# Kernel tuning notes

Measured on AMD Instinct MI355X. Metric: run time of the kernel, lower is better.

Reference implementation:

```python
import jax, jax.numpy as jnp
import numpy as np

N = 50000
E = 800000
NFEAT, NHID, NCLASS = 128, 128, 40


def setup_inputs() -> dict:
    key = jax.random.key(0)
    ks = jax.random.split(key, 8)
    x = jax.random.normal(ks[0], (N, NFEAT), dtype=jnp.float32)
    edge_index = jax.random.randint(ks[1], (2, E), 0, N, dtype=jnp.int64)
    def glorot(k, fan_in, fan_out):
        s = jnp.sqrt(6.0 / (fan_in + fan_out)).astype(jnp.float32)
        return jax.random.uniform(k, (fan_in, fan_out), jnp.float32, -s, s)
    W1 = glorot(ks[2], NFEAT, NHID); b1 = jnp.zeros((NHID,), jnp.float32)
    W2 = glorot(ks[3], NHID, NHID);  b2 = jnp.zeros((NHID,), jnp.float32)
    W3 = glorot(ks[4], NHID, NCLASS); b3 = jnp.zeros((NCLASS,), jnp.float32)
    return {"x": x, "edge_index": edge_index,
            "W1": W1, "b1": b1, "W2": W2, "b2": b2, "W3": W3, "b3": b3}


def _gcn_norm(edge_index, num_nodes, dtype):
    # Add self-loops, then symmetric normalization D^-1/2 (A+I) D^-1/2 (PyG gcn_norm).
    loop = jnp.arange(num_nodes, dtype=edge_index.dtype)
    src = jnp.concatenate([edge_index[0], loop])
    dst = jnp.concatenate([edge_index[1], loop])
    deg = jax.ops.segment_sum(jnp.ones_like(src, dtype=dtype), dst, num_segments=num_nodes)
    dinv = jnp.where(deg > 0, deg ** -0.5, 0.0).astype(dtype)
    norm = dinv[src] * dinv[dst]  # [E+N]
    return src, dst, norm


def _gcn_conv(h, src, dst, norm, W, b, num_nodes):
    h = h @ W                              # dense transform first (out_dim small)
    msg = h[src] * norm[:, None]           # gather + per-edge scale
    out = jax.ops.segment_sum(msg, dst, num_segments=num_nodes)  # scatter-add
    return out + b


def reference(x, edge_index, W1, b1, W2, b2, W3, b3):
    src, dst, norm = _gcn_norm(edge_index, N, x.dtype)
    h = jax.nn.relu(_gcn_conv(x, src, dst, norm, W1, b1, N))  # dropout: eval mode (identity)
    h = jax.nn.relu(_gcn_conv(h, src, dst, norm, W2, b2, N))
    h = _gcn_conv(h, src, dst, norm, W3, b3, N)
    return jax.nn.log_softmax(h, axis=-1)
```

## Files before the change

### kernel.cpp

```cpp
#include <hip/hip_runtime.h>
#include <stdint.h>

#define NN 50000
#define NE 800000
#define GG 782
#define NB 196
#define TT 2048
#define SB 391
#define SLAB 8192

typedef __attribute__((ext_vector_type(8))) short bfx8;
typedef __attribute__((ext_vector_type(4))) float f32x4;

__device__ inline unsigned short f2bf(float f) {
    union { float f; uint32_t u; } x; x.f = f;
    uint32_t u = x.u;
    return (unsigned short)((u + 0x7fffu + ((u >> 16) & 1u)) >> 16);
}
__device__ inline uint32_t pack2bf(float lo, float hi) {
    return (uint32_t)f2bf(lo) | ((uint32_t)f2bf(hi) << 16);
}
__device__ inline float bf2f(unsigned short h) {
    union { uint32_t u; float f; } c; c.u = ((uint32_t)h) << 16;
    return c.f;
}
__device__ inline float2 bfp2f2(uint32_t v) {
    union { uint32_t u; float f; } a, b;
    a.u = (v & 0xffffu) << 16;
    b.u = v & 0xffff0000u;
    return make_float2(a.f, b.f);
}
__device__ inline bfx8 ld8(const unsigned short* p) {
    union { uint4 u; bfx8 v; } c;
    c.u = *(const uint4*)p;
    return c.v;
}
__device__ inline bfx8 cvt8(float4 u, float4 v) {
    union { unsigned short s[8]; bfx8 r; } c;
    c.s[0] = f2bf(u.x); c.s[1] = f2bf(u.y); c.s[2] = f2bf(u.z); c.s[3] = f2bf(u.w);
    c.s[4] = f2bf(v.x); c.s[5] = f2bf(v.y); c.s[6] = f2bf(v.z); c.s[7] = f2bf(v.w);
    return c.r;
}

__global__ void prep(const float* __restrict__ W1, const float* __restrict__ W2,
                     const float* __restrict__ W3,
                     unsigned short* __restrict__ WT1, unsigned short* __restrict__ WT2,
                     unsigned short* __restrict__ WT3, int* __restrict__ cursor) {
    if (blockIdx.x == 152) {
        if (threadIdx.x < NB) cursor[threadIdx.x] = 0;
        return;
    }
    int w = blockIdx.x * 256 + threadIdx.x;
    if (w < 16384) {
        int nn = w >> 7, k = w & 127;
        WT1[nn * 128 + k] = f2bf(W1[k * 128 + nn]);
    } else if (w < 32768) {
        int w2 = w - 16384, nn = w2 >> 7, k = w2 & 127;
        WT2[nn * 128 + k] = f2bf(W2[k * 128 + nn]);
    } else if (w < 38912) {
        int w2 = w - 32768, nn = w2 >> 7, k = w2 & 127;
        WT3[nn * 128 + k] = (nn < 40) ? f2bf(W3[k * 40 + nn]) : (unsigned short)0;
    }
}

__global__ __launch_bounds__(256) void gemm1_hist(const float* __restrict__ X,
                                                  const unsigned short* __restrict__ WT,
                                                  unsigned short* __restrict__ G, int n,
                                                  const int* __restrict__ src,
                                                  const int* __restrict__ dst,
                                                  int* __restrict__ cursor,
                                                  uint32_t* __restrict__ packA, int e) {
    __shared__ int lc[NB];
    __shared__ int gb[NB];
    if (blockIdx.x >= GG) {
        int b = blockIdx.x - GG;
        int t = threadIdx.x;
        if (t < NB) lc[t] = 0;
        __syncthreads();
        int start = b * TT;
        int end = start + TT; if (end > e) end = e;
        int hi_[8], r_[8];
        uint32_t pk_[8];
#pragma unroll
        for (int j = 0; j < 8; j++) {
            int i = start + j * 256 + t;
            if (i < end) {
                int dd = dst[i], ss = src[i];
                hi_[j] = dd >> 8;
                pk_[j] = ((uint32_t)dd << 16) | (uint32_t)ss;
                r_[j] = atomicAdd(&lc[hi_[j]], 1);
            } else r_[j] = -1;
        }
        __syncthreads();
        if (t < NB) {
            int c = lc[t];
            gb[t] = c ? atomicAdd(&cursor[t], c) : 0;
        }
        __syncthreads();
#pragma unroll
        for (int j = 0; j < 8; j++) {
            if (r_[j] >= 0)
                packA[(size_t)hi_[j] * SLAB + gb[hi_[j]] + r_[j]] = pk_[j];
        }
        return;
    }
    int wave = threadIdx.x >> 6;
    int lane = threadIdx.x & 63;
    int quad = lane >> 4;
    int c = lane & 15;
    int rowbase = blockIdx.x * 64 + wave * 16;

    int arow = rowbase + c;
    if (arow >= n) arow = n - 1;
    const float* ap = X + (size_t)arow * 128 + quad * 8;
    bfx8 a[4];
#pragma unroll
    for (int kc = 0; kc < 4; kc++) {
        float4 u = *(const float4*)(ap + kc * 32);
        float4 v = *(const float4*)(ap + kc * 32 + 4);
        a[kc] = cvt8(u, v);
    }

    f32x4 acc[8];
#pragma unroll
    for (int ct = 0; ct < 8; ct++) acc[ct] = (f32x4){0.f, 0.f, 0.f, 0.f};
#pragma unroll
    for (int ct = 0; ct < 8; ct++) {
        const unsigned short* bp = WT + (size_t)(ct * 16 + c) * 128 + quad * 8;
#pragma unroll
        for (int kc = 0; kc < 4; kc++) {
            bfx8 b = ld8(bp + kc * 32);
            acc[ct] = __builtin_amdgcn_mfma_f32_16x16x32_bf16(a[kc], b, acc[ct], 0, 0, 0);
        }
    }

    int r0 = rowbase + quad * 4;
    bool odd = lane & 1;
#pragma unroll
    for (int ct = 0; ct < 8; ct++) {
        float x0 = acc[ct][0], x1 = acc[ct][1], x2 = acc[ct][2], x3 = acc[ct][3];
        float y0 = __shfl_xor(x0, 1, 64), y1 = __shfl_xor(x1, 1, 64);
        float y2 = __shfl_xor(x2, 1, 64), y3 = __shfl_xor(x3, 1, 64);
        int colp = ct * 16 + (c & ~1);
        if (!odd) {
            if (r0 + 0 < n) *(uint32_t*)(&G[(size_t)(r0 + 0) * 128 + colp]) = pack2bf(x0, y0);
            if (r0 + 1 < n) *(uint32_t*)(&G[(size_t)(r0 + 1) * 128 + colp]) = pack2bf(x1, y1);
        } else {
            if (r0 + 2 < n) *(uint32_t*)(&G[(size_t)(r0 + 2) * 128 + colp]) = pack2bf(y2, x2);
            if (r0 + 3 < n) *(uint32_t*)(&G[(size_t)(r0 + 3) * 128 + colp]) = pack2bf(y3, x3);
        }
    }
}

__global__ __launch_bounds__(256) void buildB(const uint32_t* __restrict__ packA,
                                              const int* __restrict__ cursor,
                                              int* __restrict__ row_ptr, int* __restrict__ deg,
                                              float* __restrict__ dinv,
                                              unsigned short* __restrict__ csr_src, int n) {
    __shared__ int s[256];
    __shared__ int cnt[256];
    __shared__ int rp[256];
    __shared__ int basehi, bcnt;
    int hi = blockIdx.x;
    int t = threadIdx.x;
    int bc = (t < NB) ? cursor[t] : 0;
    s[t] = bc;
    __syncthreads();
#pragma unroll
    for (int off = 1; off < 256; off <<= 1) {
        int y = (t >= off) ? s[t - off] : 0;
        __syncthreads();
        s[t] += y;
        __syncthreads();
    }
    if (t == hi) { basehi = s[t] - bc; bcnt = bc; }
    cnt[t] = 0;
    __syncthreads();
    int b0 = basehi;
    int mc = bcnt;
    const uint32_t* slab = packA + (size_t)hi * SLAB;
    for (int i = t; i < mc; i += 256)
        atomicAdd(&cnt[(slab[i] >> 16) & 0xFF], 1);
    __syncthreads();
    int v = cnt[t];
    s[t] = v;
    __syncthreads();
#pragma unroll
    for (int off = 1; off < 256; off <<= 1) {
        int y = (t >= off) ? s[t - off] : 0;
        __syncthreads();
        s[t] += y;
        __syncthreads();
    }
    rp[t] = b0 + s[t] - v;
    int node = hi * 256 + t;
    if (node < n) {
        row_ptr[node] = rp[t];
        deg[node] = v;
        dinv[node] = rsqrtf(1.0f + (float)v);
    }
    cnt[t] = 0;
    __syncthreads();
    for (int i = t; i < mc; i += 256) {
        uint32_t p = slab[i];
        int lo = (p >> 16) & 0xFF;
        int r = atomicAdd(&cnt[lo], 1);
        csr_src[rp[lo] + r] = (unsigned short)(p & 0xFFFF);
    }
}

__global__ __launch_bounds__(256) void gemm128_mfma(const unsigned short* __restrict__ A,
                                                    const unsigned short* __restrict__ WT,
                                                    const float* __restrict__ dinv,
                                                    unsigned short* __restrict__ G, int n) {
    int wave = threadIdx.x >> 6;
    int lane = threadIdx.x & 63;
    int quad = lane >> 4;
    int c = lane & 15;
    int rowbase = blockIdx.x * 64 + wave * 16;

    int arow = rowbase + c;
    if (arow >= n) arow = n - 1;
    const unsigned short* ap = A + (size_t)arow * 128 + quad * 8;
    bfx8 a[4];
#pragma unroll
    for (int kc = 0; kc < 4; kc++) a[kc] = ld8(ap + kc * 32);

    f32x4 acc[8];
#pragma unroll
    for (int ct = 0; ct < 8; ct++) acc[ct] = (f32x4){0.f, 0.f, 0.f, 0.f};
#pragma unroll
    for (int ct = 0; ct < 8; ct++) {
        const unsigned short* bp = WT + (size_t)(ct * 16 + c) * 128 + quad * 8;
#pragma unroll
        for (int kc = 0; kc < 4; kc++) {
            bfx8 b = ld8(bp + kc * 32);
            acc[ct] = __builtin_amdgcn_mfma_f32_16x16x32_bf16(a[kc], b, acc[ct], 0, 0, 0);
        }
    }

    int r0 = rowbase + quad * 4;
    float di[4];
#pragma unroll
    for (int r = 0; r < 4; r++) {
        int rr = r0 + r;
        di[r] = dinv[rr < n ? rr : 0];
    }
    bool odd = lane & 1;
#pragma unroll
    for (int ct = 0; ct < 8; ct++) {
        float x0 = acc[ct][0], x1 = acc[ct][1], x2 = acc[ct][2], x3 = acc[ct][3];
        float y0 = __shfl_xor(x0, 1, 64), y1 = __shfl_xor(x1, 1, 64);
        float y2 = __shfl_xor(x2, 1, 64), y3 = __shfl_xor(x3, 1, 64);
        int colp = ct * 16 + (c & ~1);
        if (!odd) {
            if (r0 + 0 < n) *(uint32_t*)(&G[(size_t)(r0 + 0) * 128 + colp]) = pack2bf(di[0] * x0, di[0] * y0);
            if (r0 + 1 < n) *(uint32_t*)(&G[(size_t)(r0 + 1) * 128 + colp]) = pack2bf(di[1] * x1, di[1] * y1);
        } else {
            if (r0 + 2 < n) *(uint32_t*)(&G[(size_t)(r0 + 2) * 128 + colp]) = pack2bf(di[2] * y2, di[2] * x2);
            if (r0 + 3 < n) *(uint32_t*)(&G[(size_t)(r0 + 3) * 128 + colp]) = pack2bf(di[3] * y3, di[3] * x3);
        }
    }
}

__global__ __launch_bounds__(256) void gemm40_mfma(const unsigned short* __restrict__ A,
                                                   const unsigned short* __restrict__ WT,
                                                   const float* __restrict__ dinv,
                                                   unsigned short* __restrict__ G, int n) {
    int wave = threadIdx.x >> 6;
    int lane = threadIdx.x & 63;
    int quad = lane >> 4;
    int c = lane & 15;
    int rowbase = blockIdx.x * 64 + wave * 16;

    int arow = rowbase + c;
    if (arow >= n) arow = n - 1;
    const unsigned short* ap = A + (size_t)arow * 128 + quad * 8;
    bfx8 a[4];
#pragma unroll
    for (int kc = 0; kc < 4; kc++) a[kc] = ld8(ap + kc * 32);

    f32x4 acc[3];
#pragma unroll
    for (int ct = 0; ct < 3; ct++) acc[ct] = (f32x4){0.f, 0.f, 0.f, 0.f};
#pragma unroll
    for (int ct = 0; ct < 3; ct++) {
        const unsigned short* bp = WT + (size_t)(ct * 16 + c) * 128 + quad * 8;
#pragma unroll
        for (int kc = 0; kc < 4; kc++) {
            bfx8 b = ld8(bp + kc * 32);
            acc[ct] = __builtin_amdgcn_mfma_f32_16x16x32_bf16(a[kc], b, acc[ct], 0, 0, 0);
        }
    }

    int r0 = rowbase + quad * 4;
    float di[4];
#pragma unroll
    for (int r = 0; r < 4; r++) {
        int rr = r0 + r;
        di[r] = dinv[rr < n ? rr : 0];
    }
    bool odd = lane & 1;
#pragma unroll
    for (int ct = 0; ct < 3; ct++) {
        float x0 = acc[ct][0], x1 = acc[ct][1], x2 = acc[ct][2], x3 = acc[ct][3];
        float y0 = __shfl_xor(x0, 1, 64), y1 = __shfl_xor(x1, 1, 64);
        float y2 = __shfl_xor(x2, 1, 64), y3 = __shfl_xor(x3, 1, 64);
        int colp = ct * 16 + (c & ~1);
        if (colp >= 40) continue;
        if (!odd) {
            if (r0 + 0 < n) *(uint32_t*)(&G[(size_t)(r0 + 0) * 40 + colp]) = pack2bf(di[0] * x0, di[0] * y0);
            if (r0 + 1 < n) *(uint32_t*)(&G[(size_t)(r0 + 1) * 40 + colp]) = pack2bf(di[1] * x1, di[1] * y1);
        } else {
            if (r0 + 2 < n) *(uint32_t*)(&G[(size_t)(r0 + 2) * 40 + colp]) = pack2bf(di[2] * y2, di[2] * x2);
            if (r0 + 3 < n) *(uint32_t*)(&G[(size_t)(r0 + 3) * 40 + colp]) = pack2bf(di[3] * y3, di[3] * x3);
        }
    }
}

__global__ __launch_bounds__(256) void agg128_l1(const unsigned short* __restrict__ G,
                                                 const int* __restrict__ row_ptr,
                                                 const int* __restrict__ deg,
                                                 const unsigned short* __restrict__ csr_src,
                                                 const float* __restrict__ dinv,
                                                 const float* __restrict__ b,
                                                 unsigned short* __restrict__ Y, int n) {
    int node = blockIdx.x * 4 + (threadIdx.x >> 6);
    if (node >= n) return;
    int l = threadIdx.x & 63;
    int h = l >> 5, fl = l & 31;
    const uint2* Gr = (const uint2*)G;

    float dn = dinv[node];
    float4 acc = make_float4(0.f, 0.f, 0.f, 0.f);
    if (h == 0) {
        uint2 sq = Gr[(size_t)node * 32 + fl];
        float2 a0 = bfp2f2(sq.x), a1 = bfp2f2(sq.y);
        acc = make_float4(dn * a0.x, dn * a0.y, dn * a1.x, dn * a1.y);
    }
    int p = row_ptr[node];
    int p1 = p + deg[node];
    for (int q = p; q < p1; q += 8) {
        int i0 = q + h, i1 = q + 2 + h, i2 = q + 4 + h, i3 = q + 6 + h;
        bool v0 = i0 < p1, v1 = i1 < p1, v2 = i2 < p1, v3 = i3 < p1;
        int s0 = csr_src[v0 ? i0 : p], s1 = csr_src[v1 ? i1 : p];
        int s2 = csr_src[v2 ? i2 : p], s3 = csr_src[v3 ? i3 : p];
        float d0 = v0 ? dinv[s0] : 0.f, d1 = v1 ? dinv[s1] : 0.f;
        float d2 = v2 ? dinv[s2] : 0.f, d3 = v3 ? dinv[s3] : 0.f;
        uint2 q0 = Gr[(size_t)s0 * 32 + fl], q1 = Gr[(size_t)s1 * 32 + fl];
        uint2 q2 = Gr[(size_t)s2 * 32 + fl], q3 = Gr[(size_t)s3 * 32 + fl];
        float2 x0 = bfp2f2(q0.x), y0 = bfp2f2(q0.y);
        float2 x1 = bfp2f2(q1.x), y1 = bfp2f2(q1.y);
        float2 x2 = bfp2f2(q2.x), y2 = bfp2f2(q2.y);
        float2 x3 = bfp2f2(q3.x), y3 = bfp2f2(q3.y);
        acc.x += fmaf(d0, x0.x, d1 * x1.x) + fmaf(d2, x2.x, d3 * x3.x);
        acc.y += fmaf(d0, x0.y, d1 * x1.y) + fmaf(d2, x2.y, d3 * x3.y);
        acc.z += fmaf(d0, y0.x, d1 * y1.x) + fmaf(d2, y2.x, d3 * y3.x);
        acc.w += fmaf(d0, y0.y, d1 * y1.y) + fmaf(d2, y2.y, d3 * y3.y);
    }
    acc.x += __shfl_xor(acc.x, 32, 64);
    acc.y += __shfl_xor(acc.y, 32, 64);
    acc.z += __shfl_xor(acc.z, 32, 64);
    acc.w += __shfl_xor(acc.w, 32, 64);
    float4 bb = ((const float4*)b)[fl];
    float r0 = fmaf(dn, acc.x, bb.x);
    float r1 = fmaf(dn, acc.y, bb.y);
    float r2 = fmaf(dn, acc.z, bb.z);
    float r3 = fmaf(dn, acc.w, bb.w);
    if (h == 0) {
        uint2 o;
        o.x = pack2bf(r0 > 0.f ? r0 : 0.f, r1 > 0.f ? r1 : 0.f);
        o.y = pack2bf(r2 > 0.f ? r2 : 0.f, r3 > 0.f ? r3 : 0.f);
        ((uint2*)Y)[(size_t)node * 32 + fl] = o;
    }
}

__global__ __launch_bounds__(256) void agg128(const unsigned short* __restrict__ G,
                                              const int* __restrict__ row_ptr,
                                              const int* __restrict__ deg,
                                              const unsigned short* __restrict__ csr_src,
                                              const float* __restrict__ dinv,
                                              const float* __restrict__ b,
                                              unsigned short* __restrict__ Y, int n) {
    int node = blockIdx.x * 4 + (threadIdx.x >> 6);
    if (node >= n) return;
    int l = threadIdx.x & 63;
    int h = l >> 5, fl = l & 31;
    const uint2* Gr = (const uint2*)G;

    float4 acc = make_float4(0.f, 0.f, 0.f, 0.f);
    if (h == 0) {
        uint2 sq = Gr[(size_t)node * 32 + fl];
        float2 a0 = bfp2f2(sq.x), a1 = bfp2f2(sq.y);
        acc = make_float4(a0.x, a0.y, a1.x, a1.y);
    }
    int p = row_ptr[node];
    int p1 = p + deg[node];
    for (int q = p; q < p1; q += 8) {
        int i0 = q + h, i1 = q + 2 + h, i2 = q + 4 + h, i3 = q + 6 + h;
        bool v0 = i0 < p1, v1 = i1 < p1, v2 = i2 < p1, v3 = i3 < p1;
        int s0 = csr_src[v0 ? i0 : p], s1 = csr_src[v1 ? i1 : p];
        int s2 = csr_src[v2 ? i2 : p], s3 = csr_src[v3 ? i3 : p];
        float d0 = v0 ? 1.f : 0.f, d1 = v1 ? 1.f : 0.f;
        float d2 = v2 ? 1.f : 0.f, d3 = v3 ? 1.f : 0.f;
        uint2 q0 = Gr[(size_t)s0 * 32 + fl], q1 = Gr[(size_t)s1 * 32 + fl];
        uint2 q2 = Gr[(size_t)s2 * 32 + fl], q3 = Gr[(size_t)s3 * 32 + fl];
        float2 x0 = bfp2f2(q0.x), y0 = bfp2f2(q0.y);
        float2 x1 = bfp2f2(q1.x), y1 = bfp2f2(q1.y);
        float2 x2 = bfp2f2(q2.x), y2 = bfp2f2(q2.y);
        float2 x3 = bfp2f2(q3.x), y3 = bfp2f2(q3.y);
        acc.x += fmaf(d0, x0.x, d1 * x1.x) + fmaf(d2, x2.x, d3 * x3.x);
        acc.y += fmaf(d0, x0.y, d1 * x1.y) + fmaf(d2, x2.y, d3 * x3.y);
        acc.z += fmaf(d0, y0.x, d1 * y1.x) + fmaf(d2, y2.x, d3 * y3.x);
        acc.w += fmaf(d0, y0.y, d1 * y1.y) + fmaf(d2, y2.y, d3 * y3.y);
    }
    acc.x += __shfl_xor(acc.x, 32, 64);
    acc.y += __shfl_xor(acc.y, 32, 64);
    acc.z += __shfl_xor(acc.z, 32, 64);
    acc.w += __shfl_xor(acc.w, 32, 64);
    float dn = dinv[node];
    float4 bb = ((const float4*)b)[fl];
    float r0 = fmaf(dn, acc.x, bb.x);
    float r1 = fmaf(dn, acc.y, bb.y);
    float r2 = fmaf(dn, acc.z, bb.z);
    float r3 = fmaf(dn, acc.w, bb.w);
    if (h == 0) {
        uint2 o;
        o.x = pack2bf(r0 > 0.f ? r0 : 0.f, r1 > 0.f ? r1 : 0.f);
        o.y = pack2bf(r2 > 0.f ? r2 : 0.f, r3 > 0.f ? r3 : 0.f);
        ((uint2*)Y)[(size_t)node * 32 + fl] = o;
    }
}

__global__ __launch_bounds__(256) void agg40_lsm(const unsigned short* __restrict__ G,
                                                 const int* __restrict__ row_ptr,
                                                 const int* __restrict__ deg,
                                                 const unsigned short* __restrict__ csr_src,
                                                 const float* __restrict__ dinv,
                                                 const float* __restrict__ b,
                                                 float* __restrict__ Y, int n) {
    int node = blockIdx.x * 4 + (threadIdx.x >> 6);
    if (node >= n) return;
    int l = threadIdx.x & 63;
    int h = l >> 5, fl = l & 31;
    bool act = fl < 10;
    int flc = act ? fl : 0;
    const uint2* Gr = (const uint2*)G;

    float4 acc = make_float4(0.f, 0.f, 0.f, 0.f);
    if (h == 0) {
        uint2 sq = Gr[(size_t)node * 10 + flc];
        float2 a0 = bfp2f2(sq.x), a1 = bfp2f2(sq.y);
        acc = make_float4(a0.x, a0.y, a1.x, a1.y);
    }
    int p = row_ptr[node];
    int p1 = p + deg[node];
    for (int q = p; q < p1; q += 8) {
        int i0 = q + h, i1 = q + 2 + h, i2 = q + 4 + h, i3 = q + 6 + h;
        bool v0 = i0 < p1, v1 = i1 < p1, v2 = i2 < p1, v3 = i3 < p1;
        int s0 = csr_src[v0 ? i0 : p], s1 = csr_src[v1 ? i1 : p];
        int s2 = csr_src[v2 ? i2 : p], s3 = csr_src[v3 ? i3 : p];
        float d0 = v0 ? 1.f : 0.f, d1 = v1 ? 1.f : 0.f;
        float d2 = v2 ? 1.f : 0.f, d3 = v3 ? 1.f : 0.f;
        uint2 q0 = Gr[(size_t)s0 * 10 + flc], q1 = Gr[(size_t)s1 * 10 + flc];
        uint2 q2 = Gr[(size_t)s2 * 10 + flc], q3 = Gr[(size_t)s3 * 10 + flc];
        float2 x0 = bfp2f2(q0.x), y0 = bfp2f2(q0.y);
        float2 x1 = bfp2f2(q1.x), y1 = bfp2f2(q1.y);
        float2 x2 = bfp2f2(q2.x), y2 = bfp2f2(q2.y);
        float2 x3 = bfp2f2(q3.x), y3 = bfp2f2(q3.y);
        acc.x += fmaf(d0, x0.x, d1 * x1.x) + fmaf(d2, x2.x, d3 * x3.x);
        acc.y += fmaf(d0, x0.y, d1 * x1.y) + fmaf(d2, x2.y, d3 * x3.y);
        acc.z += fmaf(d0, y0.x, d1 * y1.x) + fmaf(d2, y2.x, d3 * y3.x);
        acc.w += fmaf(d0, y0.y, d1 * y1.y) + fmaf(d2, y2.y, d3 * y3.y);
    }
    acc.x += __shfl_xor(acc.x, 32, 64);
    acc.y += __shfl_xor(acc.y, 32, 64);
    acc.z += __shfl_xor(acc.z, 32, 64);
    acc.w += __shfl_xor(acc.w, 32, 64);
    float dn = dinv[node];
    const float4* b4 = (const float4*)b;
    float4 bb = b4[flc];
    float v0_ = fmaf(dn, acc.x, bb.x);
    float v1_ = fmaf(dn, acc.y, bb.y);
    float v2_ = fmaf(dn, acc.z, bb.z);
    float v3_ = fmaf(dn, acc.w, bb.w);
    float m = act ? fmaxf(fmaxf(v0_, v1_), fmaxf(v2_, v3_)) : -1e30f;
#pragma unroll
    for (int off = 8; off > 0; off >>= 1) m = fmaxf(m, __shfl_xor(m, off, 16));
    float e0 = act ? expf(v0_ - m) : 0.f;
    float e1 = act ? expf(v1_ - m) : 0.f;
    float e2 = act ? expf(v2_ - m) : 0.f;
    float e3 = act ? expf(v3_ - m) : 0.f;
    float s_ = ((e0 + e1) + (e2 + e3));
#pragma unroll
    for (int off = 8; off > 0; off >>= 1) s_ += __shfl_xor(s_, off, 16);
    float ls = logf(s_) + m;
    if (h == 0 && act) {
        float4 o = make_float4(v0_ - ls, v1_ - ls, v2_ - ls, v3_ - ls);
        ((float4*)Y)[(size_t)node * 10 + fl] = o;
    }
}


extern "C" void kernel_launch(void* const* d_in, const int* in_sizes, int n_in,
                              void* d_out, int out_size, void* d_ws, size_t ws_size,
                              hipStream_t stream) {
    const float* x  = (const float*)d_in[0];
    const int*   ei = (const int*)d_in[1];
    const float* W1 = (const float*)d_in[2];
    const float* b1 = (const float*)d_in[3];
    const float* W2 = (const float*)d_in[4];
    const float* b2 = (const float*)d_in[5];
    const float* W3 = (const float*)d_in[6];
    const float* b3 = (const float*)d_in[7];
    float* out = (float*)d_out;

    const int n = NN, e = NE;
    const int* srcI = ei;
    const int* dstI = ei + e;

    char* ws = (char*)d_ws;
    int*            deg     = (int*)ws;
    int*            row_ptr = (int*)(ws + 200704);
    float*          dinv    = (float*)(ws + 401408);
    int*            cursor  = (int*)(ws + 602112);
    uint32_t*       packA   = (uint32_t*)(ws + 603136);
    unsigned short* csr_src = (unsigned short*)(ws + 7025664);
    unsigned short* WT1     = (unsigned short*)(ws + 8625664);
    unsigned short* WT2     = (unsigned short*)(ws + 8658432);
    unsigned short* WT3     = (unsigned short*)(ws + 8691200);
    unsigned short* bufG    = (unsigned short*)(ws + 8703488);
    unsigned short* bufA    = (unsigned short*)(ws + 21503488);

    prep<<<153, 256, 0, stream>>>(W1, W2, W3, WT1, WT2, WT3, cursor);
    gemm1_hist<<<GG + SB, 256, 0, stream>>>(x, WT1, bufG, n, srcI, dstI, cursor, packA, e);
    buildB<<<NB, 256, 0, stream>>>(packA, cursor, row_ptr, deg, dinv, csr_src, n);
    agg128_l1<<<(n + 3) / 4, 256, 0, stream>>>(bufG, row_ptr, deg, csr_src, dinv, b1, bufA, n);
    gemm128_mfma<<<GG, 256, 0, stream>>>(bufA, WT2, dinv, bufG, n);
    agg128<<<(n + 3) / 4, 256, 0, stream>>>(bufG, row_ptr, deg, csr_src, dinv, b2, bufA, n);
    gemm40_mfma<<<GG, 256, 0, stream>>>(bufA, WT3, dinv, bufG, n);
    agg40_lsm<<<(n + 3) / 4, 256, 0, stream>>>(bufG, row_ptr, deg, csr_src, dinv, b3, out, n);
}
```

Before: 271.1 us.

## Store 128-wide features in column slabs so aggregation gathers stay cache-resident

The 128-feature intermediate buffers become four 32-column slabs, each a contiguous array of 64-byte rows. The GEMMs write and read that slab layout, and the 128-wide aggregation kernels now launch four times as many blocks. Each block handles one slab for a group of nodes, interleaved so a slab's working set (about 3.2 MB) can stay in L2 during the random neighbour gathers. The cost is a fourfold re-read of the CSR indices and dinv, narrower 64-byte gathers, and a longer shuffle reduction across eight edge slots.

```diff
diff --git a/kernel.cpp b/kernel.cpp
--- a/kernel.cpp
+++ b/kernel.cpp
@@ -3,11 +3,16 @@
 
 #define NN 50000
 #define NE 800000
+#define NRP 50048
 #define GG 782
 #define NB 196
 #define TT 2048
 #define SB 391
 #define SLAB 8192
+#define SLABE (NRP * 32)
+#define SLABU (NRP * 16)
+#define SLABU2 (NRP * 8)
+#define AGGB 50000
 
 typedef __attribute__((ext_vector_type(8))) short bfx8;
 typedef __attribute__((ext_vector_type(4))) float f32x4;
@@ -136,18 +141,20 @@
 
     int r0 = rowbase + quad * 4;
     bool odd = lane & 1;
+    uint32_t* Gu = (uint32_t*)G;
 #pragma unroll
     for (int ct = 0; ct < 8; ct++) {
         float x0 = acc[ct][0], x1 = acc[ct][1], x2 = acc[ct][2], x3 = acc[ct][3];
         float y0 = __shfl_xor(x0, 1, 64), y1 = __shfl_xor(x1, 1, 64);
         float y2 = __shfl_xor(x2, 1, 64), y3 = __shfl_xor(x3, 1, 64);
         int colp = ct * 16 + (c & ~1);
+        size_t sbase = (size_t)(colp >> 5) * SLABU + ((colp & 31) >> 1);
         if (!odd) {
-            if (r0 + 0 < n) *(uint32_t*)(&G[(size_t)(r0 + 0) * 128 + colp]) = pack2bf(x0, y0);
-            if (r0 + 1 < n) *(uint32_t*)(&G[(size_t)(r0 + 1) * 128 + colp]) = pack2bf(x1, y1);
+            if (r0 + 0 < n) Gu[sbase + (size_t)(r0 + 0) * 16] = pack2bf(x0, y0);
+            if (r0 + 1 < n) Gu[sbase + (size_t)(r0 + 1) * 16] = pack2bf(x1, y1);
         } else {
-            if (r0 + 2 < n) *(uint32_t*)(&G[(size_t)(r0 + 2) * 128 + colp]) = pack2bf(y2, x2);
-            if (r0 + 3 < n) *(uint32_t*)(&G[(size_t)(r0 + 3) * 128 + colp]) = pack2bf(y3, x3);
+            if (r0 + 2 < n) Gu[sbase + (size_t)(r0 + 2) * 16] = pack2bf(y2, x2);
+            if (r0 + 3 < n) Gu[sbase + (size_t)(r0 + 3) * 16] = pack2bf(y3, x3);
         }
     }
 }
@@ -221,10 +228,10 @@
 
     int arow = rowbase + c;
     if (arow >= n) arow = n - 1;
-    const unsigned short* ap = A + (size_t)arow * 128 + quad * 8;
+    const unsigned short* ap = A + (size_t)arow * 32 + quad * 8;
     bfx8 a[4];
 #pragma unroll
-    for (int kc = 0; kc < 4; kc++) a[kc] = ld8(ap + kc * 32);
+    for (int kc = 0; kc < 4; kc++) a[kc] = ld8(ap + (size_t)kc * SLABE);
 
     f32x4 acc[8];
 #pragma unroll
@@ -247,18 +254,20 @@
         di[r] = dinv[rr < n ? rr : 0];
     }
     bool odd = lane & 1;
+    uint32_t* Gu = (uint32_t*)G;
 #pragma unroll
     for (int ct = 0; ct < 8; ct++) {
         float x0 = acc[ct][0], x1 = acc[ct][1], x2 = acc[ct][2], x3 = acc[ct][3];
         float y0 = __shfl_xor(x0, 1, 64), y1 = __shfl_xor(x1, 1, 64);
         float y2 = __shfl_xor(x2, 1, 64), y3 = __shfl_xor(x3, 1, 64);
         int colp = ct * 16 + (c & ~1);
+        size_t sbase = (size_t)(colp >> 5) * SLABU + ((colp & 31) >> 1);
         if (!odd) {
-            if (r0 + 0 < n) *(uint32_t*)(&G[(size_t)(r0 + 0) * 128 + colp]) = pack2bf(di[0] * x0, di[0] * y0);
-            if (r0 + 1 < n) *(uint32_t*)(&G[(size_t)(r0 + 1) * 128 + colp]) = pack2bf(di[1] * x1, di[1] * y1);
+            if (r0 + 0 < n) Gu[sbase + (size_t)(r0 + 0) * 16] = pack2bf(di[0] * x0, di[0] * y0);
+            if (r0 + 1 < n) Gu[sbase + (size_t)(r0 + 1) * 16] = pack2bf(di[1] * x1, di[1] * y1);
         } else {
-            if (r0 + 2 < n) *(uint32_t*)(&G[(size_t)(r0 + 2) * 128 + colp]) = pack2bf(di[2] * y2, di[2] * x2);
-            if (r0 + 3 < n) *(uint32_t*)(&G[(size_t)(r0 + 3) * 128 + colp]) = pack2bf(di[3] * y3, di[3] * x3);
+            if (r0 + 2 < n) Gu[sbase + (size_t)(r0 + 2) * 16] = pack2bf(di[2] * y2, di[2] * x2);
+            if (r0 + 3 < n) Gu[sbase + (size_t)(r0 + 3) * 16] = pack2bf(di[3] * y3, di[3] * x3);
         }
     }
 }
@@ -275,10 +284,10 @@
 
     int arow = rowbase + c;
     if (arow >= n) arow = n - 1;
-    const unsigned short* ap = A + (size_t)arow * 128 + quad * 8;
+    const unsigned short* ap = A + (size_t)arow * 32 + quad * 8;
     bfx8 a[4];
 #pragma unroll
-    for (int kc = 0; kc < 4; kc++) a[kc] = ld8(ap + kc * 32);
+    for (int kc = 0; kc < 4; kc++) a[kc] = ld8(ap + (size_t)kc * SLABE);
 
     f32x4 acc[3];
 #pragma unroll
@@ -325,53 +334,55 @@
                                                  const float* __restrict__ dinv,
                                                  const float* __restrict__ b,
                                                  unsigned short* __restrict__ Y, int n) {
-    int node = blockIdx.x * 4 + (threadIdx.x >> 6);
+    int bi = blockIdx.x;
+    int xs = bi & 7;
+    int slab = xs >> 1;
+    int grp = (bi >> 3) * 2 + (xs & 1);
+    int node = grp * 4 + (threadIdx.x >> 6);
     if (node >= n) return;
     int l = threadIdx.x & 63;
-    int h = l >> 5, fl = l & 31;
-    const uint2* Gr = (const uint2*)G;
+    int slot = l >> 3, f = l & 7;
+    const uint2* Gs = (const uint2*)G + (size_t)slab * SLABU2;
 
     float dn = dinv[node];
     float4 acc = make_float4(0.f, 0.f, 0.f, 0.f);
-    if (h == 0) {
-        uint2 sq = Gr[(size_t)node * 32 + fl];
-        float2 a0 = bfp2f2(sq.x), a1 = bfp2f2(sq.y);
-        acc = make_float4(dn * a0.x, dn * a0.y, dn * a1.x, dn * a1.y);
-    }
     int p = row_ptr[node];
     int p1 = p + deg[node];
     for (int q = p; q < p1; q += 8) {
-        int i0 = q + h, i1 = q + 2 + h, i2 = q + 4 + h, i3 = q + 6 + h;
-        bool v0 = i0 < p1, v1 = i1 < p1, v2 = i2 < p1, v3 = i3 < p1;
-        int s0 = csr_src[v0 ? i0 : p], s1 = csr_src[v1 ? i1 : p];
-        int s2 = csr_src[v2 ? i2 : p], s3 = csr_src[v3 ? i3 : p];
-        float d0 = v0 ? dinv[s0] : 0.f, d1 = v1 ? dinv[s1] : 0.f;
-        float d2 = v2 ? dinv[s2] : 0.f, d3 = v3 ? dinv[s3] : 0.f;
-        uint2 q0 = Gr[(size_t)s0 * 32 + fl], q1 = Gr[(size_t)s1 * 32 + fl];
-        uint2 q2 = Gr[(size_t)s2 * 32 + fl], q3 = Gr[(size_t)s3 * 32 + fl];
-        float2 x0 = bfp2f2(q0.x), y0 = bfp2f2(q0.y);
-        float2 x1 = bfp2f2(q1.x), y1 = bfp2f2(q1.y);
-        float2 x2 = bfp2f2(q2.x), y2 = bfp2f2(q2.y);
-        float2 x3 = bfp2f2(q3.x), y3 = bfp2f2(q3.y);
-        acc.x += fmaf(d0, x0.x, d1 * x1.x) + fmaf(d2, x2.x, d3 * x3.x);
-        acc.y += fmaf(d0, x0.y, d1 * x1.y) + fmaf(d2, x2.y, d3 * x3.y);
-        acc.z += fmaf(d0, y0.x, d1 * y1.x) + fmaf(d2, y2.x, d3 * y3.x);
-        acc.w += fmaf(d0, y0.y, d1 * y1.y) + fmaf(d2, y2.y, d3 * y3.y);
-    }
-    acc.x += __shfl_xor(acc.x, 32, 64);
-    acc.y += __shfl_xor(acc.y, 32, 64);
-    acc.z += __shfl_xor(acc.z, 32, 64);
-    acc.w += __shfl_xor(acc.w, 32, 64);
-    float4 bb = ((const float4*)b)[fl];
+        int i = q + slot;
+        bool v = i < p1;
+        int s = csr_src[v ? i : p];
+        float d = v ? dinv[s] : 0.f;
+        uint2 r = Gs[(size_t)s * 8 + f];
+        float2 lo = bfp2f2(r.x), hi = bfp2f2(r.y);
+        acc.x = fmaf(d, lo.x, acc.x);
+        acc.y = fmaf(d, lo.y, acc.y);
+        acc.z = fmaf(d, hi.x, acc.z);
+        acc.w = fmaf(d, hi.y, acc.w);
+    }
+#pragma unroll
+    for (int off = 8; off < 64; off <<= 1) {
+        acc.x += __shfl_xor(acc.x, off, 64);
+        acc.y += __shfl_xor(acc.y, off, 64);
+        acc.z += __shfl_xor(acc.z, off, 64);
+        acc.w += __shfl_xor(acc.w, off, 64);
+    }
+    uint2 sr = Gs[(size_t)node * 8 + f];
+    float2 slo = bfp2f2(sr.x), shi = bfp2f2(sr.y);
+    acc.x = fmaf(dn, slo.x, acc.x);
+    acc.y = fmaf(dn, slo.y, acc.y);
+    acc.z = fmaf(dn, shi.x, acc.z);
+    acc.w = fmaf(dn, shi.y, acc.w);
+    float4 bb = ((const float4*)b)[slab * 8 + f];
     float r0 = fmaf(dn, acc.x, bb.x);
     float r1 = fmaf(dn, acc.y, bb.y);
     float r2 = fmaf(dn, acc.z, bb.z);
     float r3 = fmaf(dn, acc.w, bb.w);
-    if (h == 0) {
+    if (slot == 0) {
         uint2 o;
         o.x = pack2bf(r0 > 0.f ? r0 : 0.f, r1 > 0.f ? r1 : 0.f);
         o.y = pack2bf(r2 > 0.f ? r2 : 0.f, r3 > 0.f ? r3 : 0.f);
-        ((uint2*)Y)[(size_t)node * 32 + fl] = o;
+        ((uint2*)Y)[(size_t)slab * SLABU2 + (size_t)node * 8 + f] = o;
     }
 }
 
@@ -382,53 +393,52 @@
                                               const float* __restrict__ dinv,
                                               const float* __restrict__ b,
                                               unsigned short* __restrict__ Y, int n) {
-    int node = blockIdx.x * 4 + (threadIdx.x >> 6);
+    int bi = blockIdx.x;
+    int xs = bi & 7;
+    int slab = xs >> 1;
+    int grp = (bi >> 3) * 2 + (xs & 1);
+    int node = grp * 4 + (threadIdx.x >> 6);
     if (node >= n) return;
     int l = threadIdx.x & 63;
-    int h = l >> 5, fl = l & 31;
-    const uint2* Gr = (const uint2*)G;
+    int slot = l >> 3, f = l & 7;
+    const uint2* Gs = (const uint2*)G + (size_t)slab * SLABU2;
 
     float4 acc = make_float4(0.f, 0.f, 0.f, 0.f);
-    if (h == 0) {
-        uint2 sq = Gr[(size_t)node * 32 + fl];
-        float2 a0 = bfp2f2(sq.x), a1 = bfp2f2(sq.y);
-        acc = make_float4(a0.x, a0.y, a1.x, a1.y);
-    }
     int p = row_ptr[node];
     int p1 = p + deg[node];
     for (int q = p; q < p1; q += 8) {
-        int i0 = q + h, i1 = q + 2 + h, i2 = q + 4 + h, i3 = q + 6 + h;
-        bool v0 = i0 < p1, v1 = i1 < p1, v2 = i2 < p1, v3 = i3 < p1;
-        int s0 = csr_src[v0 ? i0 : p], s1 = csr_src[v1 ? i1 : p];
-        int s2 = csr_src[v2 ? i2 : p], s3 = csr_src[v3 ? i3 : p];
-        float d0 = v0 ? 1.f : 0.f, d1 = v1 ? 1.f : 0.f;
-        float d2 = v2 ? 1.f : 0.f, d3 = v3 ? 1.f : 0.f;
-        uint2 q0 = Gr[(size_t)s0 * 32 + fl], q1 = Gr[(size_t)s1 * 32 + fl];
-        uint2 q2 = Gr[(size_t)s2 * 32 + fl], q3 = Gr[(size_t)s3 * 32 + fl];
-        float2 x0 = bfp2f2(q0.x), y0 = bfp2f2(q0.y);
-        float2 x1 = bfp2f2(q1.x), y1 = bfp2f2(q1.y);
-        float2 x2 = bfp2f2(q2.x), y2 = bfp2f2(q2.y);
-        float2 x3 = bfp2f2(q3.x), y3 = bfp2f2(q3.y);
-        acc.x += fmaf(d0, x0.x, d1 * x1.x) + fmaf(d2, x2.x, d3 * x3.x);
-        acc.y += fmaf(d0, x0.y, d1 * x1.y) + fmaf(d2, x2.y, d3 * x3.y);
-        acc.z += fmaf(d0, y0.x, d1 * y1.x) + fmaf(d2, y2.x, d3 * y3.x);
-        acc.w += fmaf(d0, y0.y, d1 * y1.y) + fmaf(d2, y2.y, d3 * y3.y);
-    }
-    acc.x += __shfl_xor(acc.x, 32, 64);
-    acc.y += __shfl_xor(acc.y, 32, 64);
-    acc.z += __shfl_xor(acc.z, 32, 64);
-    acc.w += __shfl_xor(acc.w, 32, 64);
+        int i = q + slot;
+        bool v = i < p1;
+        int s = csr_src[v ? i : p];
+        float d = v ? 1.f : 0.f;
+        uint2 r = Gs[(size_t)s * 8 + f];
+        float2 lo = bfp2f2(r.x), hi = bfp2f2(r.y);
+        acc.x = fmaf(d, lo.x, acc.x);
+        acc.y = fmaf(d, lo.y, acc.y);
+        acc.z = fmaf(d, hi.x, acc.z);
+        acc.w = fmaf(d, hi.y, acc.w);
+    }
+#pragma unroll
+    for (int off = 8; off < 64; off <<= 1) {
+        acc.x += __shfl_xor(acc.x, off, 64);
+        acc.y += __shfl_xor(acc.y, off, 64);
+        acc.z += __shfl_xor(acc.z, off, 64);
+        acc.w += __shfl_xor(acc.w, off, 64);
+    }
+    uint2 sr = Gs[(size_t)node * 8 + f];
+    float2 slo = bfp2f2(sr.x), shi = bfp2f2(sr.y);
+    acc.x += slo.x; acc.y += slo.y; acc.z += shi.x; acc.w += shi.y;
     float dn = dinv[node];
-    float4 bb = ((const float4*)b)[fl];
+    float4 bb = ((const float4*)b)[slab * 8 + f];
     float r0 = fmaf(dn, acc.x, bb.x);
     float r1 = fmaf(dn, acc.y, bb.y);
     float r2 = fmaf(dn, acc.z, bb.z);
     float r3 = fmaf(dn, acc.w, bb.w);
-    if (h == 0) {
+    if (slot == 0) {
         uint2 o;
         o.x = pack2bf(r0 > 0.f ? r0 : 0.f, r1 > 0.f ? r1 : 0.f);
         o.y = pack2bf(r2 > 0.f ? r2 : 0.f, r3 > 0.f ? r3 : 0.f);
-        ((uint2*)Y)[(size_t)node * 32 + fl] = o;
+        ((uint2*)Y)[(size_t)slab * SLABU2 + (size_t)node * 8 + f] = o;
     }
 }
 
@@ -530,14 +540,14 @@
     unsigned short* WT2     = (unsigned short*)(ws + 8658432);
     unsigned short* WT3     = (unsigned short*)(ws + 8691200);
     unsigned short* bufG    = (unsigned short*)(ws + 8703488);
-    unsigned short* bufA    = (unsigned short*)(ws + 21503488);
+    unsigned short* bufA    = (unsigned short*)(ws + 21515776);
 
     prep<<<153, 256, 0, stream>>>(W1, W2, W3, WT1, WT2, WT3, cursor);
     gemm1_hist<<<GG + SB, 256, 0, stream>>>(x, WT1, bufG, n, srcI, dstI, cursor, packA, e);
     buildB<<<NB, 256, 0, stream>>>(packA, cursor, row_ptr, deg, dinv, csr_src, n);
-    agg128_l1<<<(n + 3) / 4, 256, 0, stream>>>(bufG, row_ptr, deg, csr_src, dinv, b1, bufA, n);
+    agg128_l1<<<AGGB, 256, 0, stream>>>(bufG, row_ptr, deg, csr_src, dinv, b1, bufA, n);
     gemm128_mfma<<<GG, 256, 0, stream>>>(bufA, WT2, dinv, bufG, n);
-    agg128<<<(n + 3) / 4, 256, 0, stream>>>(bufG, row_ptr, deg, csr_src, dinv, b2, bufA, n);
+    agg128<<<AGGB, 256, 0, stream>>>(bufG, row_ptr, deg, csr_src, dinv, b2, bufA, n);
     gemm40_mfma<<<GG, 256, 0, stream>>>(bufA, WT3, dinv, bufG, n);
     agg40_lsm<<<(n + 3) / 4, 256, 0, stream>>>(bufG, row_ptr, deg, csr_src, dinv, b3, out, n);
 }
```

Result: slower. 357.1 us (+31.8%).

## Fold layer-1 dinv prescale into buildB and unroll agg128 to 16 edges

Applied to the files above, without the earlier changes.

The layer-1 GEMM output is now scaled in place by each node's dinv inside buildB, which already holds the per-node degrees in shared memory. This lets layer 1 reuse the generic agg128 kernel and drops the per-edge dinv[src] gathers from agg128_l1. Separately, the agg128 edge loop now issues up to 16 neighbor gathers per iteration to get more loads in flight, at the cost of more registers. It also adds an extra bf16 rounding of layer-1 features and a read-modify-write pass over them inside buildB.

```diff
diff --git a/kernel.cpp b/kernel.cpp
--- a/kernel.cpp
+++ b/kernel.cpp
@@ -156,10 +156,12 @@
                                               const int* __restrict__ cursor,
                                               int* __restrict__ row_ptr, int* __restrict__ deg,
                                               float* __restrict__ dinv,
-                                              unsigned short* __restrict__ csr_src, int n) {
+                                              unsigned short* __restrict__ csr_src,
+                                              unsigned short* __restrict__ G, int n) {
     __shared__ int s[256];
     __shared__ int cnt[256];
     __shared__ int rp[256];
+    __shared__ float sdinv[256];
     __shared__ int basehi, bcnt;
     int hi = blockIdx.x;
     int t = threadIdx.x;
@@ -193,11 +195,13 @@
         __syncthreads();
     }
     rp[t] = b0 + s[t] - v;
+    float dv = rsqrtf(1.0f + (float)v);
+    sdinv[t] = dv;
     int node = hi * 256 + t;
     if (node < n) {
         row_ptr[node] = rp[t];
         deg[node] = v;
-        dinv[node] = rsqrtf(1.0f + (float)v);
+        dinv[node] = dv;
     }
     cnt[t] = 0;
     __syncthreads();
@@ -206,6 +210,23 @@
         int lo = (p >> 16) & 0xFF;
         int r = atomicAdd(&cnt[lo], 1);
         csr_src[rp[lo] + r] = (unsigned short)(p & 0xFFFF);
+    }
+    int nbase = hi * 256;
+    int nvalid = n - nbase; if (nvalid > 256) nvalid = 256;
+    uint2* Gb = (uint2*)G + (size_t)nbase * 32;
+#pragma unroll 4
+    for (int k = 0; k < 32; k++) {
+        int idx = k * 256 + t;
+        int no = idx >> 5;
+        if (no < nvalid) {
+            uint2 vv = Gb[idx];
+            float dd = sdinv[no];
+            float2 x = bfp2f2(vv.x), y = bfp2f2(vv.y);
+            uint2 o;
+            o.x = pack2bf(dd * x.x, dd * x.y);
+            o.y = pack2bf(dd * y.x, dd * y.y);
+            Gb[idx] = o;
+        }
     }
 }
 
@@ -318,63 +339,6 @@
     }
 }
 
-__global__ __launch_bounds__(256) void agg128_l1(const unsigned short* __restrict__ G,
-                                                 const int* __restrict__ row_ptr,
-                                                 const int* __restrict__ deg,
-                                                 const unsigned short* __restrict__ csr_src,
-                                                 const float* __restrict__ dinv,
-                                                 const float* __restrict__ b,
-                                                 unsigned short* __restrict__ Y, int n) {
-    int node = blockIdx.x * 4 + (threadIdx.x >> 6);
-    if (node >= n) return;
-    int l = threadIdx.x & 63;
-    int h = l >> 5, fl = l & 31;
-    const uint2* Gr = (const uint2*)G;
-
-    float dn = dinv[node];
-    float4 acc = make_float4(0.f, 0.f, 0.f, 0.f);
-    if (h == 0) {
-        uint2 sq = Gr[(size_t)node * 32 + fl];
-        float2 a0 = bfp2f2(sq.x), a1 = bfp2f2(sq.y);
-        acc = make_float4(dn * a0.x, dn * a0.y, dn * a1.x, dn * a1.y);
-    }
-    int p = row_ptr[node];
-    int p1 = p + deg[node];
-    for (int q = p; q < p1; q += 8) {
-        int i0 = q + h, i1 = q + 2 + h, i2 = q + 4 + h, i3 = q + 6 + h;
-        bool v0 = i0 < p1, v1 = i1 < p1, v2 = i2 < p1, v3 = i3 < p1;
-        int s0 = csr_src[v0 ? i0 : p], s1 = csr_src[v1 ? i1 : p];
-        int s2 = csr_src[v2 ? i2 : p], s3 = csr_src[v3 ? i3 : p];
-        float d0 = v0 ? dinv[s0] : 0.f, d1 = v1 ? dinv[s1] : 0.f;
-        float d2 = v2 ? dinv[s2] : 0.f, d3 = v3 ? dinv[s3] : 0.f;
-        uint2 q0 = Gr[(size_t)s0 * 32 + fl], q1 = Gr[(size_t)s1 * 32 + fl];
-        uint2 q2 = Gr[(size_t)s2 * 32 + fl], q3 = Gr[(size_t)s3 * 32 + fl];
-        float2 x0 = bfp2f2(q0.x), y0 = bfp2f2(q0.y);
-        float2 x1 = bfp2f2(q1.x), y1 = bfp2f2(q1.y);
-        float2 x2 = bfp2f2(q2.x), y2 = bfp2f2(q2.y);
-        float2 x3 = bfp2f2(q3.x), y3 = bfp2f2(q3.y);
-        acc.x += fmaf(d0, x0.x, d1 * x1.x) + fmaf(d2, x2.x, d3 * x3.x);
-        acc.y += fmaf(d0, x0.y, d1 * x1.y) + fmaf(d2, x2.y, d3 * x3.y);
-        acc.z += fmaf(d0, y0.x, d1 * y1.x) + fmaf(d2, y2.x, d3 * y3.x);
-        acc.w += fmaf(d0, y0.y, d1 * y1.y) + fmaf(d2, y2.y, d3 * y3.y);
-    }
-    acc.x += __shfl_xor(acc.x, 32, 64);
-    acc.y += __shfl_xor(acc.y, 32, 64);
-    acc.z += __shfl_xor(acc.z, 32, 64);
-    acc.w += __shfl_xor(acc.w, 32, 64);
-    float4 bb = ((const float4*)b)[fl];
-    float r0 = fmaf(dn, acc.x, bb.x);
-    float r1 = fmaf(dn, acc.y, bb.y);
-    float r2 = fmaf(dn, acc.z, bb.z);
-    float r3 = fmaf(dn, acc.w, bb.w);
-    if (h == 0) {
-        uint2 o;
-        o.x = pack2bf(r0 > 0.f ? r0 : 0.f, r1 > 0.f ? r1 : 0.f);
-        o.y = pack2bf(r2 > 0.f ? r2 : 0.f, r3 > 0.f ? r3 : 0.f);
-        ((uint2*)Y)[(size_t)node * 32 + fl] = o;
-    }
-}
-
 __global__ __launch_bounds__(256) void agg128(const unsigned short* __restrict__ G,
                                               const int* __restrict__ row_ptr,
                                               const int* __restrict__ deg,
@@ -396,23 +360,48 @@
     }
     int p = row_ptr[node];
     int p1 = p + deg[node];
-    for (int q = p; q < p1; q += 8) {
+    for (int q = p; q < p1; q += 16) {
         int i0 = q + h, i1 = q + 2 + h, i2 = q + 4 + h, i3 = q + 6 + h;
         bool v0 = i0 < p1, v1 = i1 < p1, v2 = i2 < p1, v3 = i3 < p1;
         int s0 = csr_src[v0 ? i0 : p], s1 = csr_src[v1 ? i1 : p];
         int s2 = csr_src[v2 ? i2 : p], s3 = csr_src[v3 ? i3 : p];
-        float d0 = v0 ? 1.f : 0.f, d1 = v1 ? 1.f : 0.f;
-        float d2 = v2 ? 1.f : 0.f, d3 = v3 ? 1.f : 0.f;
         uint2 q0 = Gr[(size_t)s0 * 32 + fl], q1 = Gr[(size_t)s1 * 32 + fl];
         uint2 q2 = Gr[(size_t)s2 * 32 + fl], q3 = Gr[(size_t)s3 * 32 + fl];
-        float2 x0 = bfp2f2(q0.x), y0 = bfp2f2(q0.y);
-        float2 x1 = bfp2f2(q1.x), y1 = bfp2f2(q1.y);
-        float2 x2 = bfp2f2(q2.x), y2 = bfp2f2(q2.y);
-        float2 x3 = bfp2f2(q3.x), y3 = bfp2f2(q3.y);
-        acc.x += fmaf(d0, x0.x, d1 * x1.x) + fmaf(d2, x2.x, d3 * x3.x);
-        acc.y += fmaf(d0, x0.y, d1 * x1.y) + fmaf(d2, x2.y, d3 * x3.y);
-        acc.z += fmaf(d0, y0.x, d1 * y1.x) + fmaf(d2, y2.x, d3 * y3.x);
-        acc.w += fmaf(d0, y0.y, d1 * y1.y) + fmaf(d2, y2.y, d3 * y3.y);
+        bool hasB = (q + 8) < p1;
+        uint2 q4, q5, q6, q7;
+        bool v4 = false, v5 = false, v6 = false, v7 = false;
+        if (hasB) {
+            int i4 = q + 8 + h, i5 = q + 10 + h, i6 = q + 12 + h, i7 = q + 14 + h;
+            v4 = i4 < p1; v5 = i5 < p1; v6 = i6 < p1; v7 = i7 < p1;
+            int s4 = csr_src[v4 ? i4 : p], s5 = csr_src[v5 ? i5 : p];
+            int s6 = csr_src[v6 ? i6 : p], s7 = csr_src[v7 ? i7 : p];
+            q4 = Gr[(size_t)s4 * 32 + fl]; q5 = Gr[(size_t)s5 * 32 + fl];
+            q6 = Gr[(size_t)s6 * 32 + fl]; q7 = Gr[(size_t)s7 * 32 + fl];
+        }
+        {
+            float w0 = v0 ? 1.f : 0.f, w1 = v1 ? 1.f : 0.f;
+            float w2 = v2 ? 1.f : 0.f, w3 = v3 ? 1.f : 0.f;
+            float2 x0 = bfp2f2(q0.x), y0 = bfp2f2(q0.y);
+            float2 x1 = bfp2f2(q1.x), y1 = bfp2f2(q1.y);
+            float2 x2 = bfp2f2(q2.x), y2 = bfp2f2(q2.y);
+            float2 x3 = bfp2f2(q3.x), y3 = bfp2f2(q3.y);
+            acc.x += fmaf(w0, x0.x, w1 * x1.x) + fmaf(w2, x2.x, w3 * x3.x);
+            acc.y += fmaf(w0, x0.y, w1 * x1.y) + fmaf(w2, x2.y, w3 * x3.y);
+            acc.z += fmaf(w0, y0.x, w1 * y1.x) + fmaf(w2, y2.x, w3 * y3.x);
+            acc.w += fmaf(w0, y0.y, w1 * y1.y) + fmaf(w2, y2.y, w3 * y3.y);
+        }
+        if (hasB) {
+            float w4 = v4 ? 1.f : 0.f, w5 = v5 ? 1.f : 0.f;
+            float w6 = v6 ? 1.f : 0.f, w7 = v7 ? 1.f : 0.f;
+            float2 x4 = bfp2f2(q4.x), y4 = bfp2f2(q4.y);
+            float2 x5 = bfp2f2(q5.x), y5 = bfp2f2(q5.y);
+            float2 x6 = bfp2f2(q6.x), y6 = bfp2f2(q6.y);
+            float2 x7 = bfp2f2(q7.x), y7 = bfp2f2(q7.y);
+            acc.x += fmaf(w4, x4.x, w5 * x5.x) + fmaf(w6, x6.x, w7 * x7.x);
+            acc.y += fmaf(w4, x4.y, w5 * x5.y) + fmaf(w6, x6.y, w7 * x7.y);
+            acc.z += fmaf(w4, y4.x, w5 * y5.x) + fmaf(w6, y6.x, w7 * y7.x);
+            acc.w += fmaf(w4, y4.y, w5 * y5.y) + fmaf(w6, y6.y, w7 * y7.y);
+        }
     }
     acc.x += __shfl_xor(acc.x, 32, 64);
     acc.y += __shfl_xor(acc.y, 32, 64);
@@ -534,8 +523,8 @@
 
     prep<<<153, 256, 0, stream>>>(W1, W2, W3, WT1, WT2, WT3, cursor);
     gemm1_hist<<<GG + SB, 256, 0, stream>>>(x, WT1, bufG, n, srcI, dstI, cursor, packA, e);
-    buildB<<<NB, 256, 0, stream>>>(packA, cursor, row_ptr, deg, dinv, csr_src, n);
-    agg128_l1<<<(n + 3) / 4, 256, 0, stream>>>(bufG, row_ptr, deg, csr_src, dinv, b1, bufA, n);
+    buildB<<<NB, 256, 0, stream>>>(packA, cursor, row_ptr, deg, dinv, csr_src, bufG, n);
+    agg128<<<(n + 3) / 4, 256, 0, stream>>>(bufG, row_ptr, deg, csr_src, dinv, b1, bufA, n);
     gemm128_mfma<<<GG, 256, 0, stream>>>(bufA, WT2, dinv, bufG, n);
     agg128<<<(n + 3) / 4, 256, 0, stream>>>(bufG, row_ptr, deg, csr_src, dinv, b2, bufA, n);
     gemm40_mfma<<<GG, 256, 0, stream>>>(bufA, WT3, dinv, bufG, n);
```

New measurement: 279.4 us. 1.03x slower.
